# Optimization experiments

Measured on AMD Instinct MI355X. Metric: run time of the kernel, lower is better.

## Reference

```python
import jax, jax.numpy as jnp
import numpy as np
from jax import lax

PS = 2  # patch_size
DN = ('NCHW', 'OIHW', 'NCHW')


def setup_inputs() -> dict:
    key = jax.random.key(0)
    ks = jax.random.split(key, 7)
    B, C, H, W = 8, 32, 512, 512
    return {
        'x': jax.random.normal(ks[0], (B, C, H, W), dtype=jnp.float32),
        'mlp_w': jax.random.normal(ks[1], (1, 1), dtype=jnp.float32),
        'mlp_b': jax.random.normal(ks[2], (1,), dtype=jnp.float32) * 0.1,
        'conv_w': jax.random.normal(ks[3], (C, 2 * C, 1, 1), dtype=jnp.float32) * (1.0 / np.sqrt(2 * C)),
        'conv_b': jax.random.normal(ks[4], (C,), dtype=jnp.float32) * 0.1,
        'convout_w': jax.random.normal(ks[5], (C, 2, 7, 7), dtype=jnp.float32) * (1.0 / np.sqrt(2 * 49)),
        'convout_b': jax.random.normal(ks[6], (C,), dtype=jnp.float32) * 0.1,
    }


def reference(x, mlp_w, mlp_b, conv_w, conv_b, convout_w, convout_b):
    B, C, H, W = x.shape
    hn, wn = H // PS, W // PS
    # Vectorized form of the per-patch Python loop:
    # blocks: (B, C, hn, PS, wn, PS)
    xb = x.reshape(B, C, hn, PS, wn, PS)
    m = jnp.max(xb, axis=(3, 5))   # (B, C, hn, wn) patch max pool
    a = jnp.mean(xb, axis=(3, 5))  # (B, C, hn, wn) patch avg pool
    # mlp(m) + mlp(a) with shared Linear(1,1): (m + a) * w + 2b
    gate = jax.nn.sigmoid((m + a) * mlp_w[0, 0] + 2.0 * mlp_b[0])
    product = (xb * gate[:, :, :, None, :, None]).reshape(B, C, H, W)
    # channel attention block
    cat = jnp.concatenate([product, x], axis=1)  # (B, 2C, H, W)
    out = lax.conv_general_dilated(cat, conv_w, (1, 1), 'SAME',
                                   dimension_numbers=DN) + conv_b[None, :, None, None]
    fs = out
    cm = jnp.max(out, axis=1, keepdims=True)   # channel max pool (B,1,H,W)
    ca = jnp.mean(out, axis=1, keepdims=True)  # channel avg pool (B,1,H,W)
    att = lax.conv_general_dilated(jnp.concatenate([cm, ca], axis=1), convout_w,
                                   (1, 1), 'SAME', dimension_numbers=DN)
    att = att + convout_b[None, :, None, None]
    return jax.nn.sigmoid(att) * fs
```

## Files before the change

kernel.cpp:

```cpp
#include <hip/hip_runtime.h>
#include <cstdint>
#include <cstddef>

constexpr int B = 8, C = 32, H = 512, W = 512;
constexpr int HW = H * W;

__device__ __forceinline__ float sigmoidf_(float z) {
    return 1.0f / (1.0f + __expf(-z));
}

__global__ __launch_bounds__(256, 4) void k1_gate_conv(
    const float* __restrict__ x, const float* __restrict__ mlp_w,
    const float* __restrict__ mlp_b, const float* __restrict__ conv_w,
    const float* __restrict__ conv_b, float* __restrict__ fs,
    float* __restrict__ cm, float* __restrict__ ca)
{
    __shared__ float xs[32][256];
    __shared__ float gs[32][64];
    const int t  = threadIdx.x;
    const int c0 = blockIdx.x * 128;
    const int h0 = blockIdx.y * 2;
    const int b  = blockIdx.z;

    #pragma unroll
    for (int k = 0; k < 8; ++k) {
        int li = k * 256 + t;
        int c = li >> 6, q = li & 63;
        int p = q * 4;
        int row = p >> 7, col = p & 127;
        const float4 v = *(const float4*)(x + ((size_t)(b * C + c) * H + h0 + row) * W + c0 + col);
        *(float4*)&xs[c][p] = v;
    }
    __syncthreads();

    const float gw = mlp_w[0];
    const float gb = 2.0f * mlp_b[0];
    #pragma unroll
    for (int k = 0; k < 8; ++k) {
        int gi = k * 256 + t;
        int c = gi >> 6, wp = gi & 63;
        float a0 = xs[c][2 * wp],       a1 = xs[c][2 * wp + 1];
        float a2 = xs[c][128 + 2 * wp], a3 = xs[c][129 + 2 * wp];
        float mx = fmaxf(fmaxf(a0, a1), fmaxf(a2, a3));
        float av = 0.25f * ((a0 + a1) + (a2 + a3));
        gs[c][wp] = sigmoidf_(fmaf(mx + av, gw, gb));
    }
    __syncthreads();

    const int row = t >> 7, col = t & 127, wp = col >> 1;
    float xv[32], xg[32];
    #pragma unroll
    for (int c = 0; c < 32; ++c) {
        float v = xs[c][t];
        xv[c] = v;
        xg[c] = v * gs[c][wp];
    }
    float cmax = -3.4e38f, csum = 0.0f;
    const size_t pixoff = ((size_t)(b * C) * H + h0 + row) * W + c0 + col;
    #pragma unroll 4
    for (int o = 0; o < 32; ++o) {
        const float* wr = conv_w + o * 64;
        float acc0 = conv_b[o], acc1 = 0.0f;
        #pragma unroll
        for (int c = 0; c < 32; ++c) {
            acc0 = fmaf(xg[c], wr[c],      acc0);
            acc1 = fmaf(xv[c], wr[32 + c], acc1);
        }
        float acc = acc0 + acc1;
        fs[pixoff + (size_t)o * HW] = acc;
        cmax = fmaxf(cmax, acc);
        csum += acc;
    }
    const size_t pp = ((size_t)b * H + h0 + row) * W + c0 + col;
    cm[pp] = cmax;
    ca[pp] = csum * (1.0f / 32.0f);
}

__global__ __launch_bounds__(256, 4) void k2_conv7_sigmul(
    const float* __restrict__ cm, const float* __restrict__ ca,
    const float* __restrict__ convout_w, const float* __restrict__ convout_b,
    float* __restrict__ io )
{
    __shared__ float sm[2][10][264];
    const int t  = threadIdx.x;
    const int x0 = blockIdx.x * 256;
    const int y0 = blockIdx.y * 4;
    const int b  = blockIdx.z;

    for (int idx = t; idx < 2 * 10 * 264; idx += 256) {
        int j   = idx / (10 * 264);
        int rem = idx - j * (10 * 264);
        int r   = rem / 264;
        int cc  = rem - r * 264;
        int gy = y0 - 3 + r;
        int gx = x0 - 3 + cc;
        const float* P = j ? ca : cm;
        float v = 0.0f;
        if (cc < 262 && (unsigned)gy < (unsigned)H && (unsigned)gx < (unsigned)W)
            v = P[(size_t)b * HW + (size_t)gy * W + gx];
        sm[j][r][cc] = v;
    }
    __syncthreads();

    const int ty  = t >> 6;
    const int tx4 = (t & 63) * 4;

    #pragma unroll 1
    for (int oc = 0; oc < 4; ++oc) {
        const int ob = oc * 8;
        float acc[8][4];
        #pragma unroll
        for (int o = 0; o < 8; ++o) {
            float bb = convout_b[ob + o];
            #pragma unroll
            for (int px = 0; px < 4; ++px) acc[o][px] = bb;
        }
        #pragma unroll 1
        for (int j = 0; j < 2; ++j) {
            #pragma unroll
            for (int dy = 0; dy < 7; ++dy) {
                const float* rp = &sm[j][ty + dy][tx4];
                float4 va = *(const float4*)&rp[0];
                float4 vb = *(const float4*)&rp[4];
                float2 vc = *(const float2*)&rp[8];
                float v[10] = {va.x, va.y, va.z, va.w,
                               vb.x, vb.y, vb.z, vb.w, vc.x, vc.y};
                #pragma unroll
                for (int dx = 0; dx < 7; ++dx) {
                    #pragma unroll
                    for (int o = 0; o < 8; ++o) {
                        float wv = convout_w[((ob + o) * 2 + j) * 49 + dy * 7 + dx];
                        #pragma unroll
                        for (int px = 0; px < 4; ++px)
                            acc[o][px] = fmaf(v[dx + px], wv, acc[o][px]);
                    }
                }
            }
        }
        #pragma unroll
        for (int o = 0; o < 8; ++o) {
            const size_t base = ((size_t)(b * C + ob + o) * H + y0 + ty) * W + x0 + tx4;
            float4 f = *(const float4*)&io[base];
            float4 r;
            r.x = f.x * sigmoidf_(acc[o][0]);
            r.y = f.y * sigmoidf_(acc[o][1]);
            r.z = f.z * sigmoidf_(acc[o][2]);
            r.w = f.w * sigmoidf_(acc[o][3]);
            *(float4*)&io[base] = r;
        }
    }
}

extern "C" void kernel_launch(void* const* d_in, const int* in_sizes, int n_in,
                              void* d_out, int out_size, void* d_ws, size_t ws_size,
                              hipStream_t stream)
{
    const float* x         = (const float*)d_in[0];
    const float* mlp_w     = (const float*)d_in[1];
    const float* mlp_b     = (const float*)d_in[2];
    const float* conv_w    = (const float*)d_in[3];
    const float* conv_b    = (const float*)d_in[4];
    const float* convout_w = (const float*)d_in[5];
    const float* convout_b = (const float*)d_in[6];

    float* out = (float*)d_out;
    float* cm  = (float*)d_ws;
    float* ca  = cm + (size_t)B * HW;

    k1_gate_conv<<<dim3(4, 256, 8), 256, 0, stream>>>(
        x, mlp_w, mlp_b, conv_w, conv_b, out, cm, ca);
    k2_conv7_sigmul<<<dim3(2, 128, 8), 256, 0, stream>>>(
        cm, ca, convout_w, convout_b, out);
}
```

Baseline: 658.6 us.

## Run the 7x7 attention conv on bf16 MFMA with split-precision hi/lo terms

Rewrites the second kernel so the 7x7 spatial convolution over the channel max/avg maps runs on 32x32x16 bf16 matrix instructions instead of scalar FMAs. The input window and the weights are each split into high and low bf16 parts, and three MFMAs per row approximate fp32 accuracy. Tiling becomes 128x8 pixels per block with per-lane shifted loads from LDS. The cost targeted is the scalar-ALU bound conv. In exchange the sigmoid-multiply writeback is now scalar and strided across channels rather than float4, and the split-bf16 scheme adds a small precision risk.

```diff
diff --git a/kernel.cpp b/kernel.cpp
--- a/kernel.cpp
+++ b/kernel.cpp
@@ -8,6 +8,17 @@
 __device__ __forceinline__ float sigmoidf_(float z) {
     return 1.0f / (1.0f + __expf(-z));
 }
+
+__device__ __forceinline__ unsigned short bf16rne(float x) {
+    unsigned int b = __float_as_uint(x);
+    return (unsigned short)((b + 0x7FFFu + ((b >> 16) & 1u)) >> 16);
+}
+__device__ __forceinline__ float bf16tof(unsigned short h) {
+    return __uint_as_float(((unsigned int)h) << 16);
+}
+
+typedef short s8v  __attribute__((ext_vector_type(8)));
+typedef float f16v __attribute__((ext_vector_type(16)));
 
 __global__ __launch_bounds__(256, 4) void k1_gate_conv(
     const float* __restrict__ x, const float* __restrict__ mlp_w,
@@ -76,77 +87,104 @@
     ca[pp] = csum * (1.0f / 32.0f);
 }
 
-__global__ __launch_bounds__(256, 4) void k2_conv7_sigmul(
+__global__ __launch_bounds__(256, 3) void k2_conv7_mfma(
     const float* __restrict__ cm, const float* __restrict__ ca,
     const float* __restrict__ convout_w, const float* __restrict__ convout_b,
     float* __restrict__ io )
 {
-    __shared__ float sm[2][10][264];
+    __shared__ unsigned short win[4 * 14 * 144];
     const int t  = threadIdx.x;
-    const int x0 = blockIdx.x * 256;
-    const int y0 = blockIdx.y * 4;
+    const int x0 = blockIdx.x * 128;
+    const int y0 = blockIdx.y * 8;
     const int b  = blockIdx.z;
 
-    for (int idx = t; idx < 2 * 10 * 264; idx += 256) {
-        int j   = idx / (10 * 264);
-        int rem = idx - j * (10 * 264);
-        int r   = rem / 264;
-        int cc  = rem - r * 264;
-        int gy = y0 - 3 + r;
-        int gx = x0 - 3 + cc;
-        const float* P = j ? ca : cm;
-        float v = 0.0f;
-        if (cc < 262 && (unsigned)gy < (unsigned)H && (unsigned)gx < (unsigned)W)
-            v = P[(size_t)b * HW + (size_t)gy * W + gx];
-        sm[j][r][cc] = v;
-    }
+    #pragma unroll
+    for (int k = 0; k < 16; ++k) {
+        int n = k * 256 + t;
+        if (n < 4032) {
+            int j   = (n >= 2016) ? 1 : 0;
+            int rem = n - j * 2016;
+            int row = rem / 144;
+            int col = rem - row * 144;
+            int gy = y0 - 3 + row;
+            int gx = x0 - 3 + col;
+            float v = 0.0f;
+            if ((unsigned)gy < (unsigned)H && (unsigned)gx < (unsigned)W)
+                v = (j ? ca : cm)[(size_t)b * HW + (size_t)gy * W + gx];
+            unsigned short hb = bf16rne(v);
+            unsigned short lb = bf16rne(v - bf16tof(hb));
+            win[n]        = hb;
+            win[n + 4032] = lb;
+        }
+    }
+
+    const int l  = t & 63;
+    const int wv = t >> 6;
+    const int o  = l & 31;
+    const int j  = l >> 5;
+    s8v whi[7], wlo[7];
+    #pragma unroll
+    for (int dy = 0; dy < 7; ++dy) {
+        #pragma unroll
+        for (int q = 0; q < 8; ++q) {
+            float wf = (q < 7) ? convout_w[(o * 2 + j) * 49 + dy * 7 + q] : 0.0f;
+            unsigned short hb = bf16rne(wf);
+            unsigned short lb = bf16rne(wf - bf16tof(hb));
+            whi[dy][q] = (short)hb;
+            wlo[dy][q] = (short)lb;
+        }
+    }
+    float bias[16];
+    #pragma unroll
+    for (int r = 0; r < 16; ++r)
+        bias[r] = convout_b[(r & 3) + 8 * (r >> 2) + 4 * j];
     __syncthreads();
 
-    const int ty  = t >> 6;
-    const int tx4 = (t & 63) * 4;
+    const int xl  = wv * 32 + o;
+    const int q0  = xl >> 1;
+    const bool odd = (xl & 1) != 0;
 
     #pragma unroll 1
-    for (int oc = 0; oc < 4; ++oc) {
-        const int ob = oc * 8;
-        float acc[8][4];
-        #pragma unroll
-        for (int o = 0; o < 8; ++o) {
-            float bb = convout_b[ob + o];
-            #pragma unroll
-            for (int px = 0; px < 4; ++px) acc[o][px] = bb;
-        }
-        #pragma unroll 1
-        for (int j = 0; j < 2; ++j) {
-            #pragma unroll
-            for (int dy = 0; dy < 7; ++dy) {
-                const float* rp = &sm[j][ty + dy][tx4];
-                float4 va = *(const float4*)&rp[0];
-                float4 vb = *(const float4*)&rp[4];
-                float2 vc = *(const float2*)&rp[8];
-                float v[10] = {va.x, va.y, va.z, va.w,
-                               vb.x, vb.y, vb.z, vb.w, vc.x, vc.y};
-                #pragma unroll
-                for (int dx = 0; dx < 7; ++dx) {
-                    #pragma unroll
-                    for (int o = 0; o < 8; ++o) {
-                        float wv = convout_w[((ob + o) * 2 + j) * 49 + dy * 7 + dx];
-                        #pragma unroll
-                        for (int px = 0; px < 4; ++px)
-                            acc[o][px] = fmaf(v[dx + px], wv, acc[o][px]);
-                    }
-                }
+    for (int y = 0; y < 8; ++y) {
+        f16v acc;
+        #pragma unroll
+        for (int r = 0; r < 16; ++r) acc[r] = bias[r];
+
+        #pragma unroll
+        for (int dy = 0; dy < 7; ++dy) {
+            const unsigned int* rp =
+                (const unsigned int*)win + (size_t)(y + dy) * 72 + j * 1008 + q0;
+            unsigned int d0 = rp[0], d1 = rp[1], d2 = rp[2], d3 = rp[3], d4 = rp[4];
+            const unsigned int* rp2 = rp + 2016;
+            unsigned int e0 = rp2[0], e1 = rp2[1], e2 = rp2[2], e3 = rp2[3], e4 = rp2[4];
+
+            union { unsigned int u[4]; s8v s; } Bh, Bl;
+            if (odd) {
+                Bh.u[0] = (d0 >> 16) | (d1 << 16);
+                Bh.u[1] = (d1 >> 16) | (d2 << 16);
+                Bh.u[2] = (d2 >> 16) | (d3 << 16);
+                Bh.u[3] = (d3 >> 16) | (d4 << 16);
+                Bl.u[0] = (e0 >> 16) | (e1 << 16);
+                Bl.u[1] = (e1 >> 16) | (e2 << 16);
+                Bl.u[2] = (e2 >> 16) | (e3 << 16);
+                Bl.u[3] = (e3 >> 16) | (e4 << 16);
+            } else {
+                Bh.u[0] = d0; Bh.u[1] = d1; Bh.u[2] = d2; Bh.u[3] = d3;
+                Bl.u[0] = e0; Bl.u[1] = e1; Bl.u[2] = e2; Bl.u[3] = e3;
             }
-        }
-        #pragma unroll
-        for (int o = 0; o < 8; ++o) {
-            const size_t base = ((size_t)(b * C + ob + o) * H + y0 + ty) * W + x0 + tx4;
-            float4 f = *(const float4*)&io[base];
-            float4 r;
-            r.x = f.x * sigmoidf_(acc[o][0]);
-            r.y = f.y * sigmoidf_(acc[o][1]);
-            r.z = f.z * sigmoidf_(acc[o][2]);
-            r.w = f.w * sigmoidf_(acc[o][3]);
-            *(float4*)&io[base] = r;
+            acc = __builtin_amdgcn_mfma_f32_32x32x16_bf16(whi[dy], Bh.s, acc, 0, 0, 0);
+            acc = __builtin_amdgcn_mfma_f32_32x32x16_bf16(whi[dy], Bl.s, acc, 0, 0, 0);
+            acc = __builtin_amdgcn_mfma_f32_32x32x16_bf16(wlo[dy], Bh.s, acc, 0, 0, 0);
+        }
+
+        const int Y = y0 + y;
+        const int X = x0 + xl;
+        #pragma unroll
+        for (int r = 0; r < 16; ++r) {
+            int oc = (r & 3) + 8 * (r >> 2) + 4 * j;
+            size_t a = ((size_t)(b * C + oc) * H + Y) * W + X;
+            float f = io[a];
+            io[a] = f * sigmoidf_(acc[r]);
         }
     }
 }
@@ -169,6 +207,6 @@
 
     k1_gate_conv<<<dim3(4, 256, 8), 256, 0, stream>>>(
         x, mlp_w, mlp_b, conv_w, conv_b, out, cm, ca);
-    k2_conv7_sigmul<<<dim3(2, 128, 8), 256, 0, stream>>>(
+    k2_conv7_mfma<<<dim3(4, 64, 8), 256, 0, stream>>>(
         cm, ca, convout_w, convout_b, out);
 }
```

Measured after the change: 616.4 us. 1.07x faster.
